# Kernel tuning notes

Hardware: AMD Instinct MI355X
Metric: run time of the kernel (lower is better)

The kernel has to match this reference:

```python
import jax, jax.numpy as jnp
import numpy as np

D_MODEL = 1024
NUM_HEADS = 16
D_HEAD = D_MODEL // NUM_HEADS
SCALE = float(np.sqrt(D_HEAD))
NEG = -1e9


def setup_inputs() -> dict:
    key = jax.random.key(0)
    ks = jax.random.split(key, 4)
    B, K = 4, 1024
    tokens = jax.random.normal(ks[0], (B, K, D_MODEL), dtype=jnp.float32)
    token_mask = jnp.ones((B, K), dtype=jnp.int32)
    W_qkv = jax.random.normal(ks[1], (D_MODEL, 3 * D_MODEL), dtype=jnp.float32) * 0.02
    b_qkv = jnp.zeros((3 * D_MODEL,), dtype=jnp.float32)
    W_proj = jax.random.normal(ks[2], (D_MODEL, D_MODEL), dtype=jnp.float32) * 0.02
    b_proj = jnp.zeros((D_MODEL,), dtype=jnp.float32)
    return {"tokens": tokens, "token_mask": token_mask, "W_qkv": W_qkv,
            "b_qkv": b_qkv, "W_proj": W_proj, "b_proj": b_proj}


def reference(tokens, token_mask, W_qkv, b_qkv, W_proj, b_proj):
    B, K, D = tokens.shape
    H, dh = NUM_HEADS, D // NUM_HEADS
    # QKV projection: (B, K, 3D) -> (3, B, H, K, dh)
    qkv = (tokens @ W_qkv + b_qkv).reshape(B, K, 3, H, dh)
    qkv = jnp.transpose(qkv, (2, 0, 3, 1, 4))
    q, k, v = qkv[0], qkv[1], qkv[2]
    # scaled scores (B, H, K, K)
    attn = jnp.einsum('bhqd,bhkd->bhqk', q, k) / SCALE
    # additive padding mask: valid iff both query and key positions valid
    tm = token_mask.astype(attn.dtype)
    m = tm[:, None, None, :] * tm[:, None, :, None]          # (B,1,K,K)
    attn = attn + (1.0 - jnp.clip(m, 0.0)) * NEG
    attn = jax.nn.softmax(attn, axis=-1)
    # weighted values, merge heads
    out = jnp.einsum('bhqk,bhkd->bhqd', attn, v)
    out = jnp.transpose(out, (0, 2, 1, 3)).reshape(B, K, D)
    out = out @ W_proj + b_proj
    tokens_out = tokens + out                                 # residual (dropout=0)
    attn_out = attn.mean(axis=1)                              # (B, K, K)
    return tokens_out, attn_out
```

## Files before the change

### kernel.cpp

```cpp
#include <hip/hip_runtime.h>
#include <hip/hip_bf16.h>
#include <math.h>

#define SEQ   1024
#define DM    1024
#define NH    16
#define DH    64
#define INV_SCALE 0.125f
#define NEGBIG   -1e9f
#define MASKPEN 80.0f

typedef __attribute__((ext_vector_type(8))) __bf16 bf16x8;
typedef __attribute__((ext_vector_type(4))) float floatx4;
typedef unsigned short ushort_t;

__device__ __forceinline__ floatx4 mfma16(bf16x8 a, bf16x8 b, floatx4 c) {
    return __builtin_amdgcn_mfma_f32_16x16x32_bf16(a, b, c, 0, 0, 0);
}

__device__ __forceinline__ ushort_t f2bf(float f) {
    unsigned int u = __float_as_uint(f);
    u += 0x7fffu + ((u >> 16) & 1u);
    return (ushort_t)(u >> 16);
}

__device__ __forceinline__ void gload_lds16(const void* g, void* l) {
    __builtin_amdgcn_global_load_lds(
        (const __attribute__((address_space(1))) unsigned int*)g,
        (__attribute__((address_space(3))) unsigned int*)l, 16, 0, 0);
}

__global__ __launch_bounds__(256) void k_prep(const float* __restrict__ tokens,
                                              ushort_t* __restrict__ Xbf,
                                              const float* __restrict__ Wqkv,
                                              ushort_t* __restrict__ Wt,
                                              const float* __restrict__ Wproj,
                                              ushort_t* __restrict__ Wpt) {
    __shared__ ushort_t tile[32][33];
    int bxg = blockIdx.x;
    if (bxg < 2048) {
        int i = (bxg * 256 + threadIdx.x) * 8;
        float4 a = *(const float4*)(tokens + i);
        float4 b = *(const float4*)(tokens + i + 4);
        union { ushort_t s[8]; uint4 v; } pk;
        pk.s[0] = f2bf(a.x); pk.s[1] = f2bf(a.y); pk.s[2] = f2bf(a.z); pk.s[3] = f2bf(a.w);
        pk.s[4] = f2bf(b.x); pk.s[5] = f2bf(b.y); pk.s[6] = f2bf(b.z); pk.s[7] = f2bf(b.w);
        *(uint4*)(Xbf + i) = pk.v;
        return;
    }
    const float* src; ushort_t* dst; int R, C, bx, by;
    if (bxg < 5120) {
        int idx = bxg - 2048;
        src = Wqkv; dst = Wt; R = DM; C = 3 * DM;
        bx = (idx % 96) * 32; by = (idx / 96) * 32;
    } else {
        int idx = bxg - 5120;
        src = Wproj; dst = Wpt; R = DM; C = DM;
        bx = (idx % 32) * 32; by = (idx / 32) * 32;
    }
    int tx = threadIdx.x & 31, ty = threadIdx.x >> 5;
    for (int i = ty; i < 32; i += 8)
        tile[i][tx] = f2bf(src[(size_t)(by + i) * C + bx + tx]);
    __syncthreads();
    for (int i = ty; i < 32; i += 8)
        dst[(size_t)(bx + i) * R + by + tx] = tile[tx][i];
}

__device__ __forceinline__ void gemm128_single(const ushort_t* __restrict__ A,
                                               const ushort_t* __restrict__ Bt,
                                               int m0, int n0, int Kd,
                                               floatx4 acc[4][4], ushort_t* smem) {
    int tid  = threadIdx.x;
    int wave = tid >> 6, lane = tid & 63;
    int l15 = lane & 15, quad = lane >> 4;
    int wr = (wave >> 1) * 64, wc = (wave & 1) * 64;
    int rsub = lane >> 2;
    int ksub = (((lane & 3) ^ ((lane >> 3) & 3)) * 8);
    int rsw  = (l15 >> 1) & 3;

    for (int k0 = 0; k0 < Kd; k0 += 32) {
        __syncthreads();
        #pragma unroll
        for (int c = 0; c < 2; ++c) {
            int rbase = wave * 32 + c * 16;
            gload_lds16(A  + (size_t)(m0 + rbase + rsub) * Kd + k0 + ksub,
                        smem + rbase * 32);
            gload_lds16(Bt + (size_t)(n0 + rbase + rsub) * Kd + k0 + ksub,
                        smem + 4096 + rbase * 32);
        }
        __syncthreads();

        bf16x8 af[4], bfr[4];
        #pragma unroll
        for (int i = 0; i < 4; ++i)
            af[i] = *(const bf16x8*)(smem + (wr + i * 16 + l15) * 32 + (quad ^ rsw) * 8);
        #pragma unroll
        for (int j = 0; j < 4; ++j)
            bfr[j] = *(const bf16x8*)(smem + 4096 + (wc + j * 16 + l15) * 32 + (quad ^ rsw) * 8);
        #pragma unroll
        for (int i = 0; i < 4; ++i)
            #pragma unroll
            for (int j = 0; j < 4; ++j)
                acc[i][j] = mfma16(af[i], bfr[j], acc[i][j]);
    }
}

__device__ __forceinline__ void gemm128_dbuf(const ushort_t* __restrict__ A,
                                             const ushort_t* __restrict__ Bt,
                                             int m0, int n0, int Kd,
                                             floatx4 acc[4][4], ushort_t* smem) {
    int tid  = threadIdx.x;
    int wave = tid >> 6, lane = tid & 63;
    int l15 = lane & 15, quad = lane >> 4;
    int wr = (wave >> 1) * 64, wc = (wave & 1) * 64;
    int rsub = lane >> 2;
    int ksub = (((lane & 3) ^ ((lane >> 3) & 3)) * 8);
    int rsw  = (l15 >> 1) & 3;

    #pragma unroll
    for (int c = 0; c < 2; ++c) {
        int rbase = wave * 32 + c * 16;
        gload_lds16(A  + (size_t)(m0 + rbase + rsub) * Kd + ksub,
                    smem + rbase * 32);
        gload_lds16(Bt + (size_t)(n0 + rbase + rsub) * Kd + ksub,
                    smem + 4096 + rbase * 32);
    }

    for (int k0 = 0; k0 < Kd; k0 += 32) {
        int sel = (k0 >> 5) & 1;
        ushort_t* cur = smem + sel * 8192;
        __syncthreads();
        if (k0 + 32 < Kd) {
            ushort_t* nxt = smem + (sel ^ 1) * 8192;
            #pragma unroll
            for (int c = 0; c < 2; ++c) {
                int rbase = wave * 32 + c * 16;
                gload_lds16(A  + (size_t)(m0 + rbase + rsub) * Kd + (k0 + 32) + ksub,
                            nxt + rbase * 32);
                gload_lds16(Bt + (size_t)(n0 + rbase + rsub) * Kd + (k0 + 32) + ksub,
                            nxt + 4096 + rbase * 32);
            }
        }

        bf16x8 af[4], bfr[4];
        #pragma unroll
        for (int i = 0; i < 4; ++i)
            af[i] = *(const bf16x8*)(cur + (wr + i * 16 + l15) * 32 + (quad ^ rsw) * 8);
        #pragma unroll
        for (int j = 0; j < 4; ++j)
            bfr[j] = *(const bf16x8*)(cur + 4096 + (wc + j * 16 + l15) * 32 + (quad ^ rsw) * 8);
        #pragma unroll
        for (int i = 0; i < 4; ++i)
            #pragma unroll
            for (int j = 0; j < 4; ++j)
                acc[i][j] = mfma16(af[i], bfr[j], acc[i][j]);
    }
}

__global__ __launch_bounds__(256, 2) void k_qkv_gemm(const ushort_t* __restrict__ X,
                                                     const ushort_t* __restrict__ Wt,
                                                     const float* __restrict__ bias,
                                                     ushort_t* __restrict__ qb,
                                                     ushort_t* __restrict__ kb,
                                                     ushort_t* __restrict__ vtb) {
    __shared__ ushort_t smem[16384];
    int m0 = blockIdx.y * 128, n0 = blockIdx.x * 128;
    floatx4 acc[4][4];
    #pragma unroll
    for (int i = 0; i < 4; ++i)
        #pragma unroll
        for (int j = 0; j < 4; ++j) acc[i][j] = (floatx4)0.0f;

    gemm128_dbuf(X, Wt, m0, n0, DM, acc, smem);

    int tid = threadIdx.x, wave = tid >> 6, lane = tid & 63;
    int l15 = lane & 15, quad = lane >> 4;
    int wr = (wave >> 1) * 64, wc = (wave & 1) * 64;
    #pragma unroll
    for (int i = 0; i < 4; ++i) {
        int mrow0 = m0 + wr + i * 16 + quad * 4;
        int b = mrow0 >> 10, t0 = mrow0 & 1023;
        #pragma unroll
        for (int j = 0; j < 4; ++j) {
            int n = n0 + wc + j * 16 + l15;
            float bv = bias[n];
            int sec = n >> 10, nn = n & 1023;
            int h = nn >> 6, d = nn & 63;
            if (sec == 2) {
                union { ushort_t s[4]; uint2 v; } pk;
                #pragma unroll
                for (int r = 0; r < 4; ++r) pk.s[r] = f2bf(acc[i][j][r] + bv);
                *(uint2*)(vtb + (((size_t)(b * NH + h) * DH + d) * SEQ + t0)) = pk.v;
            } else {
                ushort_t* dst = (sec == 0) ? qb : kb;
                #pragma unroll
                for (int r = 0; r < 4; ++r)
                    dst[((size_t)(b * NH + h) * SEQ + t0 + r) * DH + d] =
                        f2bf(acc[i][j][r] + bv);
            }
        }
    }
}

__global__ __launch_bounds__(256, 4) void k_attn_flash(const ushort_t* __restrict__ qb,
                                                       const ushort_t* __restrict__ kb,
                                                       const ushort_t* __restrict__ vtb,
                                                       const int* __restrict__ mask,
                                                       float* __restrict__ lbuf,
                                                       ushort_t* __restrict__ ob) {
    __shared__ ushort_t ks[2 * 64 * 64];
    __shared__ ushort_t vs[2 * 64 * 64];
    __shared__ ushort_t ps[4 * 16 * 64];
    int bh = blockIdx.x, qt = blockIdx.y;
    int b = bh >> 4, h = bh & 15;
    int tid = threadIdx.x, wave = tid >> 6, lane = tid & 63;
    int l15 = lane & 15, quad = lane >> 4;
    int qrow = qt * 64 + wave * 16;
    ushort_t* pw = ps + wave * 1024;
    int sw7 = l15 & 7;

    int srow = wave * 16 + (lane >> 3);
    int slog = (lane & 7) ^ (srow & 7);

    const ushort_t* qbase = qb + ((size_t)bh * SEQ + qrow + l15) * DH;
    bf16x8 aq0 = *(const bf16x8*)(qbase + quad * 8);
    bf16x8 aq1 = *(const bf16x8*)(qbase + 32 + quad * 8);

    bf16x8 vones;
    #pragma unroll
    for (int i = 0; i < 8; ++i) vones[i] = (__bf16)1.0f;

    float qp[4];
    #pragma unroll
    for (int r = 0; r < 4; ++r)
        qp[r] = MASKPEN * (float)mask[b * SEQ + qrow + quad * 4 + r];

    floatx4 oacc[4], lacc = (floatx4)0.0f;
    #pragma unroll
    for (int t = 0; t < 4; ++t) oacc[t] = (floatx4)0.0f;

    #pragma unroll
    for (int c = 0; c < 2; ++c) {
        gload_lds16(kb  + ((size_t)bh * SEQ + srow + c * 8) * DH + slog * 8,
                    ks + (wave * 16 + c * 8) * 64);
        gload_lds16(vtb + ((size_t)bh * DH + srow + c * 8) * SEQ + slog * 8,
                    vs + (wave * 16 + c * 8) * 64);
    }

    for (int it = 0; it < SEQ / 64; ++it) {
        int kc = it * 64;
        int sel = it & 1;
        __syncthreads();
        if (it + 1 < SEQ / 64) {
            int nsel = sel ^ 1;
            #pragma unroll
            for (int c = 0; c < 2; ++c) {
                gload_lds16(kb  + ((size_t)bh * SEQ + kc + 64 + srow + c * 8) * DH + slog * 8,
                            ks + nsel * 4096 + (wave * 16 + c * 8) * 64);
                gload_lds16(vtb + ((size_t)bh * DH + srow + c * 8) * SEQ + kc + 64 + slog * 8,
                            vs + nsel * 4096 + (wave * 16 + c * 8) * 64);
            }
        }
        const ushort_t* kcur = ks + sel * 4096;
        const ushort_t* vcur = vs + sel * 4096;

        floatx4 s[4];
        #pragma unroll
        for (int j = 0; j < 4; ++j) {
            int row = j * 16 + l15;
            bf16x8 k0 = *(const bf16x8*)(kcur + row * 64 + ((quad ^ sw7) * 8));
            bf16x8 k1 = *(const bf16x8*)(kcur + row * 64 + (((quad + 4) ^ sw7) * 8));
            s[j] = mfma16(aq0, k0, (floatx4)0.0f);
            s[j] = mfma16(aq1, k1, s[j]);
        }
        #pragma unroll
        for (int j = 0; j < 4; ++j) {
            float km = (float)mask[b * SEQ + kc + j * 16 + l15];
            #pragma unroll
            for (int r = 0; r < 4; ++r) {
                float arg = s[j][r] * INV_SCALE + (qp[r] * km - MASKPEN);
                float p = __expf(arg);
                int rd = quad * 4 + r;
                int ch = (2 * j + (l15 >> 3)) ^ (rd & 7);
                pw[rd * 64 + ch * 8 + (l15 & 7)] = f2bf(p);
            }
        }
        bf16x8 pa0 = *(const bf16x8*)(pw + l15 * 64 + ((quad ^ sw7) * 8));
        bf16x8 pa1 = *(const bf16x8*)(pw + l15 * 64 + (((quad + 4) ^ sw7) * 8));
        lacc = mfma16(pa0, vones, lacc);
        lacc = mfma16(pa1, vones, lacc);
        #pragma unroll
        for (int t = 0; t < 4; ++t) {
            bf16x8 bv0 = *(const bf16x8*)(vcur + (t * 16 + l15) * 64 + ((quad ^ sw7) * 8));
            bf16x8 bv1 = *(const bf16x8*)(vcur + (t * 16 + l15) * 64 + (((quad + 4) ^ sw7) * 8));
            oacc[t] = mfma16(pa0, bv0, oacc[t]);
            oacc[t] = mfma16(pa1, bv1, oacc[t]);
        }
    }
    float invl[4];
    #pragma unroll
    for (int r = 0; r < 4; ++r) invl[r] = 1.0f / lacc[r];
    #pragma unroll
    for (int t = 0; t < 4; ++t)
        #pragma unroll
        for (int r = 0; r < 4; ++r)
            ob[((size_t)b * SEQ + qrow + quad * 4 + r) * DM + h * DH + t * 16 + l15] =
                f2bf(oacc[t][r] * invl[r]);
    if (l15 == 0) {
        #pragma unroll
        for (int r = 0; r < 4; ++r)
            lbuf[(size_t)bh * SEQ + qrow + quad * 4 + r] = invl[r];
    }
}

__device__ __forceinline__ void proj_body(const ushort_t* __restrict__ ob,
                                          const ushort_t* __restrict__ Wpt,
                                          const float* __restrict__ bias,
                                          const float* __restrict__ tokens,
                                          float* __restrict__ out,
                                          int m0, int n0, ushort_t* smem) {
    floatx4 acc[4][4];
    #pragma unroll
    for (int i = 0; i < 4; ++i)
        #pragma unroll
        for (int j = 0; j < 4; ++j) acc[i][j] = (floatx4)0.0f;

    gemm128_single(ob, Wpt, m0, n0, DM, acc, smem);

    int tid = threadIdx.x, wave = tid >> 6, lane = tid & 63;
    int l15 = lane & 15, quad = lane >> 4;
    int wr = (wave >> 1) * 64, wc = (wave & 1) * 64;
    #pragma unroll
    for (int i = 0; i < 4; ++i) {
        int m0r = m0 + wr + i * 16 + quad * 4;
        #pragma unroll
        for (int j = 0; j < 4; ++j) {
            int n = n0 + wc + j * 16 + l15;
            float bv = bias[n];
            #pragma unroll
            for (int r = 0; r < 4; ++r) {
                size_t idx = (size_t)(m0r + r) * DM + n;
                out[idx] = acc[i][j][r] + bv + tokens[idx];
            }
        }
    }
}

__device__ __forceinline__ void avg_body(const ushort_t* __restrict__ qb,
                                         const ushort_t* __restrict__ kb,
                                         const int* __restrict__ mask,
                                         const float* __restrict__ lbuf,
                                         float* __restrict__ attn_out,
                                         int b, int qt, int kt, ushort_t* ks) {
    int tid = threadIdx.x, wave = tid >> 6, lane = tid & 63;
    int l15 = lane & 15, quad = lane >> 4;
    int q0 = qt * 64 + wave * 16;
    int kbase = kt * 64;
    int sw7 = l15 & 7;

    int srow = wave * 16 + (lane >> 3);
    int slog = (lane & 7) ^ (srow & 7);
    int bh0 = b * NH;

    float qp[4], km[4];
    #pragma unroll
    for (int r = 0; r < 4; ++r)
        qp[r] = MASKPEN * (float)mask[b * SEQ + q0 + quad * 4 + r];
    #pragma unroll
    for (int j = 0; j < 4; ++j)
        km[j] = (float)mask[b * SEQ + kbase + j * 16 + l15];

    floatx4 aacc[4];
    #pragma unroll
    for (int j = 0; j < 4; ++j) aacc[j] = (floatx4)0.0f;

    #pragma unroll
    for (int c = 0; c < 2; ++c)
        gload_lds16(kb + ((size_t)bh0 * SEQ + kbase + srow + c * 8) * DH + slog * 8,
                    ks + (wave * 16 + c * 8) * 64);
    const ushort_t* qp0 = qb + ((size_t)bh0 * SEQ + q0 + l15) * DH;
    bf16x8 aq0 = *(const bf16x8*)(qp0 + quad * 8);
    bf16x8 aq1 = *(const bf16x8*)(qp0 + 32 + quad * 8);
    floatx4 il = *(const floatx4*)(lbuf + (size_t)bh0 * SEQ + q0 + quad * 4);
    __syncthreads();

    for (int h = 0; h < NH; ++h) {
        ushort_t* cur = ks + (h & 1) * 4096;
        ushort_t* nxt = ks + ((h + 1) & 1) * 4096;
        if (h + 1 < NH) {
            #pragma unroll
            for (int c = 0; c < 2; ++c)
                gload_lds16(kb + ((size_t)(bh0 + h + 1) * SEQ + kbase + srow + c * 8) * DH + slog * 8,
                            nxt + (wave * 16 + c * 8) * 64);
        }
        bf16x8 caq0 = aq0, caq1 = aq1;
        floatx4 cil = il;
        if (h + 1 < NH) {
            const ushort_t* qpn = qb + ((size_t)(bh0 + h + 1) * SEQ + q0 + l15) * DH;
            aq0 = *(const bf16x8*)(qpn + quad * 8);
            aq1 = *(const bf16x8*)(qpn + 32 + quad * 8);
            il = *(const floatx4*)(lbuf + (size_t)(bh0 + h + 1) * SEQ + q0 + quad * 4);
        }
        cil *= 0.0625f;

        #pragma unroll
        for (int j = 0; j < 4; ++j) {
            int row = j * 16 + l15;
            bf16x8 k0 = *(const bf16x8*)(cur + row * 64 + ((quad ^ sw7) * 8));
            bf16x8 k1 = *(const bf16x8*)(cur + row * 64 + (((quad + 4) ^ sw7) * 8));
            floatx4 s = mfma16(caq0, k0, (floatx4)0.0f);
            s = mfma16(caq1, k1, s);
            #pragma unroll
            for (int r = 0; r < 4; ++r) {
                float arg = s[r] * INV_SCALE + (qp[r] * km[j] - MASKPEN);
                aacc[j][r] += __expf(arg) * cil[r];
            }
        }
        __syncthreads();
    }
    #pragma unroll
    for (int j = 0; j < 4; ++j)
        #pragma unroll
        for (int r = 0; r < 4; ++r)
            attn_out[((size_t)b * SEQ + q0 + quad * 4 + r) * SEQ +
                     kbase + j * 16 + l15] = aacc[j][r];
}

__global__ __launch_bounds__(256, 2) void k_proj_avg(const ushort_t* __restrict__ ob,
                                                     const ushort_t* __restrict__ Wpt,
                                                     const float* __restrict__ bias,
                                                     const float* __restrict__ tokens,
                                                     float* __restrict__ out,
                                                     const ushort_t* __restrict__ qb,
                                                     const ushort_t* __restrict__ kb,
                                                     const int* __restrict__ mask,
                                                     const float* __restrict__ lbuf,
                                                     float* __restrict__ attn_out) {
    __shared__ ushort_t smem[8192];
    int bxg = blockIdx.x;
    if (bxg < 256) {
        int xcd = bxg & 7, rank = bxg >> 3;
        int m = xcd * 4 + (rank >> 3);
        int n = rank & 7;
        proj_body(ob, Wpt, bias, tokens, out, m * 128, n * 128, smem);
    } else {
        int i = bxg - 256;
        int xcd = i & 7, rank = i >> 3;
        int b = rank >> 5;
        int r2 = rank & 31;
        int qt = (xcd >> 1) * 4 + (r2 >> 3);
        int kt = (xcd & 1) * 8 + (r2 & 7);
        avg_body(qb, kb, mask, lbuf, attn_out, b, qt, kt, smem);
    }
}

__global__ __launch_bounds__(256, 2) void k_proj(const ushort_t* __restrict__ ob,
                                                 const ushort_t* __restrict__ Wpt,
                                                 const float* __restrict__ bias,
                                                 const float* __restrict__ tokens,
                                                 float* __restrict__ out) {
    __shared__ ushort_t smem[8192];
    proj_body(ob, Wpt, bias, tokens, out, blockIdx.y * 128, blockIdx.x * 128, smem);
}

__global__ __launch_bounds__(256, 4) void k_attn_avg(const ushort_t* __restrict__ qb,
                                                     const ushort_t* __restrict__ kb,
                                                     const int* __restrict__ mask,
                                                     const float* __restrict__ lbuf,
                                                     float* __restrict__ attn_out) {
    __shared__ ushort_t ks[2 * 64 * 64];
    int i = blockIdx.x;
    int xcd = i & 7, rank = i >> 3;
    int b = rank >> 5;
    int r2 = rank & 31;
    int qt = (xcd >> 1) * 4 + (r2 >> 3);
    int kt = (xcd & 1) * 8 + (r2 & 7);
    avg_body(qb, kb, mask, lbuf, attn_out, b, qt, kt, ks);
}

extern "C" void kernel_launch(void* const* d_in, const int* in_sizes, int n_in,
                              void* d_out, int out_size, void* d_ws, size_t ws_size,
                              hipStream_t stream) {
    const float* tokens = (const float*)d_in[0];
    const int*   mask   = (const int*)d_in[1];
    const float* Wqkv   = (const float*)d_in[2];
    const float* bqkv   = (const float*)d_in[3];
    const float* Wproj  = (const float*)d_in[4];
    const float* bproj  = (const float*)d_in[5];

    float* out_tok  = (float*)d_out;
    float* out_attn = out_tok + (size_t)4 * SEQ * SEQ;

    ushort_t* Wt   = (ushort_t*)d_ws;
    ushort_t* Wpt  = Wt  + (size_t)3 * DM * DM;
    ushort_t* qbuf = Wpt + (size_t)DM * DM;
    ushort_t* kbuf = qbuf + (size_t)4 * SEQ * DM;
    ushort_t* vtb  = kbuf + (size_t)4 * SEQ * DM;
    float*    lbuf = (float*)(vtb + (size_t)4 * SEQ * DM);
    ushort_t* obuf_ws = (ushort_t*)(lbuf + (size_t)4 * NH * SEQ);
    const size_t WS_NEED = 42205184;

    bool big_ws = ws_size >= WS_NEED;
    ushort_t* Xbf  = (ushort_t*)out_attn;
    ushort_t* obuf = big_ws ? obuf_ws
                            : (ushort_t*)(out_attn + (size_t)2 * SEQ * SEQ);

    k_prep<<<6144, 256, 0, stream>>>(tokens, Xbf, Wqkv, Wt, Wproj, Wpt);
    k_qkv_gemm<<<dim3(24, 32), 256, 0, stream>>>(Xbf, Wt, bqkv, qbuf, kbuf, vtb);
    k_attn_flash<<<dim3(64, 16), 256, 0, stream>>>(qbuf, kbuf, vtb, mask, lbuf, obuf);
    if (big_ws) {
        k_proj_avg<<<256 + 1024, 256, 0, stream>>>(obuf, Wpt, bproj, tokens, out_tok,
                                                   qbuf, kbuf, mask, lbuf, out_attn);
    } else {
        k_proj<<<dim3(8, 32), 256, 0, stream>>>(obuf, Wpt, bproj, tokens, out_tok);
        k_attn_avg<<<1024, 256, 0, stream>>>(qbuf, kbuf, mask, lbuf, out_attn);
    }
}
```

Before: 199.0 us.

## Split fused proj/avg kernel and pipeline projection GEMM with 4-stage LDS buffering

Replaces the combined projection+attention-average kernel with separate launches, and rewrites the output projection GEMM as a standalone kernel using a 4-deep LDS ring buffer with explicit vmcnt waits so global loads for three future K-tiles are in flight during MFMA work. The XCD-aware tile mapping is kept. The intent is to hide load latency in the projection GEMM, which previously synced twice per K-step with a single buffer. The cost is 64KB of LDS per block (occupancy 1), and losing the concurrent overlap of projection and averaging blocks within one launch.

```diff
diff --git a/kernel.cpp b/kernel.cpp
--- a/kernel.cpp
+++ b/kernel.cpp
@@ -66,45 +66,6 @@
         dst[(size_t)(bx + i) * R + by + tx] = tile[tx][i];
 }
 
-__device__ __forceinline__ void gemm128_single(const ushort_t* __restrict__ A,
-                                               const ushort_t* __restrict__ Bt,
-                                               int m0, int n0, int Kd,
-                                               floatx4 acc[4][4], ushort_t* smem) {
-    int tid  = threadIdx.x;
-    int wave = tid >> 6, lane = tid & 63;
-    int l15 = lane & 15, quad = lane >> 4;
-    int wr = (wave >> 1) * 64, wc = (wave & 1) * 64;
-    int rsub = lane >> 2;
-    int ksub = (((lane & 3) ^ ((lane >> 3) & 3)) * 8);
-    int rsw  = (l15 >> 1) & 3;
-
-    for (int k0 = 0; k0 < Kd; k0 += 32) {
-        __syncthreads();
-        #pragma unroll
-        for (int c = 0; c < 2; ++c) {
-            int rbase = wave * 32 + c * 16;
-            gload_lds16(A  + (size_t)(m0 + rbase + rsub) * Kd + k0 + ksub,
-                        smem + rbase * 32);
-            gload_lds16(Bt + (size_t)(n0 + rbase + rsub) * Kd + k0 + ksub,
-                        smem + 4096 + rbase * 32);
-        }
-        __syncthreads();
-
-        bf16x8 af[4], bfr[4];
-        #pragma unroll
-        for (int i = 0; i < 4; ++i)
-            af[i] = *(const bf16x8*)(smem + (wr + i * 16 + l15) * 32 + (quad ^ rsw) * 8);
-        #pragma unroll
-        for (int j = 0; j < 4; ++j)
-            bfr[j] = *(const bf16x8*)(smem + 4096 + (wc + j * 16 + l15) * 32 + (quad ^ rsw) * 8);
-        #pragma unroll
-        for (int i = 0; i < 4; ++i)
-            #pragma unroll
-            for (int j = 0; j < 4; ++j)
-                acc[i][j] = mfma16(af[i], bfr[j], acc[i][j]);
-    }
-}
-
 __device__ __forceinline__ void gemm128_dbuf(const ushort_t* __restrict__ A,
                                              const ushort_t* __restrict__ Bt,
                                              int m0, int n0, int Kd,
@@ -313,23 +274,75 @@
     }
 }
 
-__device__ __forceinline__ void proj_body(const ushort_t* __restrict__ ob,
-                                          const ushort_t* __restrict__ Wpt,
-                                          const float* __restrict__ bias,
-                                          const float* __restrict__ tokens,
-                                          float* __restrict__ out,
-                                          int m0, int n0, ushort_t* smem) {
-    floatx4 acc[4][4];
-    #pragma unroll
-    for (int i = 0; i < 4; ++i)
-        #pragma unroll
-        for (int j = 0; j < 4; ++j) acc[i][j] = (floatx4)0.0f;
-
-    gemm128_single(ob, Wpt, m0, n0, DM, acc, smem);
-
-    int tid = threadIdx.x, wave = tid >> 6, lane = tid & 63;
+__device__ __forceinline__ void proj_stage(const ushort_t* __restrict__ ob,
+                                           const ushort_t* __restrict__ Wpt,
+                                           int m0, int n0, int t,
+                                           int wave, int rsub, int ksub,
+                                           ushort_t* buf) {
+    #pragma unroll
+    for (int c = 0; c < 2; ++c) {
+        int rbase = wave * 32 + c * 16;
+        gload_lds16(ob  + (size_t)(m0 + rbase + rsub) * DM + t * 32 + ksub,
+                    buf + rbase * 32);
+        gload_lds16(Wpt + (size_t)(n0 + rbase + rsub) * DM + t * 32 + ksub,
+                    buf + 4096 + rbase * 32);
+    }
+}
+
+__global__ __launch_bounds__(256, 1) void k_proj(const ushort_t* __restrict__ ob,
+                                                 const ushort_t* __restrict__ Wpt,
+                                                 const float* __restrict__ bias,
+                                                 const float* __restrict__ tokens,
+                                                 float* __restrict__ out) {
+    __shared__ ushort_t smem[4 * 8192];
+    int bxg = blockIdx.x;
+    int xcd = bxg & 7, rank = bxg >> 3;
+    int m0 = (xcd * 4 + (rank >> 3)) * 128;
+    int n0 = (rank & 7) * 128;
+
+    int tid  = threadIdx.x;
+    int wave = tid >> 6, lane = tid & 63;
     int l15 = lane & 15, quad = lane >> 4;
     int wr = (wave >> 1) * 64, wc = (wave & 1) * 64;
+    int rsub = lane >> 2;
+    int ksub = (((lane & 3) ^ ((lane >> 3) & 3)) * 8);
+    int rsw  = (l15 >> 1) & 3;
+
+    floatx4 acc[4][4];
+    #pragma unroll
+    for (int i = 0; i < 4; ++i)
+        #pragma unroll
+        for (int j = 0; j < 4; ++j) acc[i][j] = (floatx4)0.0f;
+
+    proj_stage(ob, Wpt, m0, n0, 0, wave, rsub, ksub, smem);
+    proj_stage(ob, Wpt, m0, n0, 1, wave, rsub, ksub, smem + 8192);
+    proj_stage(ob, Wpt, m0, n0, 2, wave, rsub, ksub, smem + 16384);
+
+    for (int t = 0; t < 32; ++t) {
+        __builtin_amdgcn_s_barrier();
+        if (t + 3 < 32)
+            proj_stage(ob, Wpt, m0, n0, t + 3, wave, rsub, ksub,
+                       smem + ((t + 3) & 3) * 8192);
+        if (t < 29)       asm volatile("s_waitcnt vmcnt(12)" ::: "memory");
+        else if (t == 29) asm volatile("s_waitcnt vmcnt(8)"  ::: "memory");
+        else if (t == 30) asm volatile("s_waitcnt vmcnt(4)"  ::: "memory");
+        else              asm volatile("s_waitcnt vmcnt(0)"  ::: "memory");
+
+        const ushort_t* cur = smem + (t & 3) * 8192;
+        bf16x8 af[4], bfr[4];
+        #pragma unroll
+        for (int i = 0; i < 4; ++i)
+            af[i] = *(const bf16x8*)(cur + (wr + i * 16 + l15) * 32 + (quad ^ rsw) * 8);
+        #pragma unroll
+        for (int j = 0; j < 4; ++j)
+            bfr[j] = *(const bf16x8*)(cur + 4096 + (wc + j * 16 + l15) * 32 + (quad ^ rsw) * 8);
+        #pragma unroll
+        for (int i = 0; i < 4; ++i)
+            #pragma unroll
+            for (int j = 0; j < 4; ++j)
+                acc[i][j] = mfma16(af[i], bfr[j], acc[i][j]);
+    }
+
     #pragma unroll
     for (int i = 0; i < 4; ++i) {
         int m0r = m0 + wr + i * 16 + quad * 4;
@@ -424,43 +437,6 @@
         for (int r = 0; r < 4; ++r)
             attn_out[((size_t)b * SEQ + q0 + quad * 4 + r) * SEQ +
                      kbase + j * 16 + l15] = aacc[j][r];
-}
-
-__global__ __launch_bounds__(256, 2) void k_proj_avg(const ushort_t* __restrict__ ob,
-                                                     const ushort_t* __restrict__ Wpt,
-                                                     const float* __restrict__ bias,
-                                                     const float* __restrict__ tokens,
-                                                     float* __restrict__ out,
-                                                     const ushort_t* __restrict__ qb,
-                                                     const ushort_t* __restrict__ kb,
-                                                     const int* __restrict__ mask,
-                                                     const float* __restrict__ lbuf,
-                                                     float* __restrict__ attn_out) {
-    __shared__ ushort_t smem[8192];
-    int bxg = blockIdx.x;
-    if (bxg < 256) {
-        int xcd = bxg & 7, rank = bxg >> 3;
-        int m = xcd * 4 + (rank >> 3);
-        int n = rank & 7;
-        proj_body(ob, Wpt, bias, tokens, out, m * 128, n * 128, smem);
-    } else {
-        int i = bxg - 256;
-        int xcd = i & 7, rank = i >> 3;
-        int b = rank >> 5;
-        int r2 = rank & 31;
-        int qt = (xcd >> 1) * 4 + (r2 >> 3);
-        int kt = (xcd & 1) * 8 + (r2 & 7);
-        avg_body(qb, kb, mask, lbuf, attn_out, b, qt, kt, smem);
-    }
-}
-
-__global__ __launch_bounds__(256, 2) void k_proj(const ushort_t* __restrict__ ob,
-                                                 const ushort_t* __restrict__ Wpt,
-                                                 const float* __restrict__ bias,
-                                                 const float* __restrict__ tokens,
-                                                 float* __restrict__ out) {
-    __shared__ ushort_t smem[8192];
-    proj_body(ob, Wpt, bias, tokens, out, blockIdx.y * 128, blockIdx.x * 128, smem);
 }
 
 __global__ __launch_bounds__(256, 4) void k_attn_avg(const ushort_t* __restrict__ qb,
@@ -508,11 +484,6 @@
     k_prep<<<6144, 256, 0, stream>>>(tokens, Xbf, Wqkv, Wt, Wproj, Wpt);
     k_qkv_gemm<<<dim3(24, 32), 256, 0, stream>>>(Xbf, Wt, bqkv, qbuf, kbuf, vtb);
     k_attn_flash<<<dim3(64, 16), 256, 0, stream>>>(qbuf, kbuf, vtb, mask, lbuf, obuf);
-    if (big_ws) {
-        k_proj_avg<<<256 + 1024, 256, 0, stream>>>(obuf, Wpt, bproj, tokens, out_tok,
-                                                   qbuf, kbuf, mask, lbuf, out_attn);
-    } else {
-        k_proj<<<dim3(8, 32), 256, 0, stream>>>(obuf, Wpt, bproj, tokens, out_tok);
-        k_attn_avg<<<1024, 256, 0, stream>>>(qbuf, kbuf, mask, lbuf, out_attn);
-    }
-}
+    k_proj<<<256, 256, 0, stream>>>(obuf, Wpt, bproj, tokens, out_tok);
+    k_attn_avg<<<1024, 256, 0, stream>>>(qbuf, kbuf, mask, lbuf, out_attn);
+}
```

Measured after the change: 200.4 us. No clear change (+0.7%).

## Deepen QKV GEMM LDS pipeline to four stages with explicit vmcnt waits

Applied to the files above, without the earlier changes.

Replaces the double-buffered QKV GEMM main loop with a 4-buffer ring that keeps three k-tiles of global-to-LDS loads in flight. It uses explicit s_waitcnt vmcnt counts and a raw s_barrier instead of __syncthreads. The goal is to hide more global memory latency behind MFMA work. LDS per block doubles to 64KB, which may limit occupancy at two blocks per CU, and the hand-tuned vmcnt counts rely on each stage issuing exactly four loads per thread.

```diff
diff --git a/kernel.cpp b/kernel.cpp
--- a/kernel.cpp
+++ b/kernel.cpp
@@ -105,10 +105,30 @@
     }
 }
 
-__device__ __forceinline__ void gemm128_dbuf(const ushort_t* __restrict__ A,
-                                             const ushort_t* __restrict__ Bt,
-                                             int m0, int n0, int Kd,
-                                             floatx4 acc[4][4], ushort_t* smem) {
+__device__ __forceinline__ void qkv_stage(const ushort_t* __restrict__ X,
+                                          const ushort_t* __restrict__ Wt,
+                                          int m0, int n0, int t,
+                                          int wave, int rsub, int ksub,
+                                          ushort_t* buf) {
+    #pragma unroll
+    for (int c = 0; c < 2; ++c) {
+        int rbase = wave * 32 + c * 16;
+        gload_lds16(X  + (size_t)(m0 + rbase + rsub) * DM + t * 32 + ksub,
+                    buf + rbase * 32);
+        gload_lds16(Wt + (size_t)(n0 + rbase + rsub) * DM + t * 32 + ksub,
+                    buf + 4096 + rbase * 32);
+    }
+}
+
+__global__ __launch_bounds__(256, 2) void k_qkv_gemm(const ushort_t* __restrict__ X,
+                                                     const ushort_t* __restrict__ Wt,
+                                                     const float* __restrict__ bias,
+                                                     ushort_t* __restrict__ qb,
+                                                     ushort_t* __restrict__ kb,
+                                                     ushort_t* __restrict__ vtb) {
+    __shared__ ushort_t smem[4 * 8192];
+    int m0 = blockIdx.y * 128, n0 = blockIdx.x * 128;
+
     int tid  = threadIdx.x;
     int wave = tid >> 6, lane = tid & 63;
     int l15 = lane & 15, quad = lane >> 4;
@@ -117,31 +137,26 @@
     int ksub = (((lane & 3) ^ ((lane >> 3) & 3)) * 8);
     int rsw  = (l15 >> 1) & 3;
 
-    #pragma unroll
-    for (int c = 0; c < 2; ++c) {
-        int rbase = wave * 32 + c * 16;
-        gload_lds16(A  + (size_t)(m0 + rbase + rsub) * Kd + ksub,
-                    smem + rbase * 32);
-        gload_lds16(Bt + (size_t)(n0 + rbase + rsub) * Kd + ksub,
-                    smem + 4096 + rbase * 32);
-    }
-
-    for (int k0 = 0; k0 < Kd; k0 += 32) {
-        int sel = (k0 >> 5) & 1;
-        ushort_t* cur = smem + sel * 8192;
-        __syncthreads();
-        if (k0 + 32 < Kd) {
-            ushort_t* nxt = smem + (sel ^ 1) * 8192;
-            #pragma unroll
-            for (int c = 0; c < 2; ++c) {
-                int rbase = wave * 32 + c * 16;
-                gload_lds16(A  + (size_t)(m0 + rbase + rsub) * Kd + (k0 + 32) + ksub,
-                            nxt + rbase * 32);
-                gload_lds16(Bt + (size_t)(n0 + rbase + rsub) * Kd + (k0 + 32) + ksub,
-                            nxt + 4096 + rbase * 32);
-            }
-        }
-
+    floatx4 acc[4][4];
+    #pragma unroll
+    for (int i = 0; i < 4; ++i)
+        #pragma unroll
+        for (int j = 0; j < 4; ++j) acc[i][j] = (floatx4)0.0f;
+
+    qkv_stage(X, Wt, m0, n0, 0, wave, rsub, ksub, smem);
+    qkv_stage(X, Wt, m0, n0, 1, wave, rsub, ksub, smem + 8192);
+    qkv_stage(X, Wt, m0, n0, 2, wave, rsub, ksub, smem + 16384);
+
+    for (int t = 0; t < 32; ++t) {
+        if (t < 30)       asm volatile("s_waitcnt vmcnt(8)" ::: "memory");
+        else if (t == 30) asm volatile("s_waitcnt vmcnt(4)" ::: "memory");
+        else              asm volatile("s_waitcnt vmcnt(0)" ::: "memory");
+        __builtin_amdgcn_s_barrier();
+        if (t + 3 < 32)
+            qkv_stage(X, Wt, m0, n0, t + 3, wave, rsub, ksub,
+                      smem + ((t + 3) & 3) * 8192);
+
+        const ushort_t* cur = smem + (t & 3) * 8192;
         bf16x8 af[4], bfr[4];
         #pragma unroll
         for (int i = 0; i < 4; ++i)
@@ -155,27 +170,7 @@
             for (int j = 0; j < 4; ++j)
                 acc[i][j] = mfma16(af[i], bfr[j], acc[i][j]);
     }
-}
-
-__global__ __launch_bounds__(256, 2) void k_qkv_gemm(const ushort_t* __restrict__ X,
-                                                     const ushort_t* __restrict__ Wt,
-                                                     const float* __restrict__ bias,
-                                                     ushort_t* __restrict__ qb,
-                                                     ushort_t* __restrict__ kb,
-                                                     ushort_t* __restrict__ vtb) {
-    __shared__ ushort_t smem[16384];
-    int m0 = blockIdx.y * 128, n0 = blockIdx.x * 128;
-    floatx4 acc[4][4];
-    #pragma unroll
-    for (int i = 0; i < 4; ++i)
-        #pragma unroll
-        for (int j = 0; j < 4; ++j) acc[i][j] = (floatx4)0.0f;
-
-    gemm128_dbuf(X, Wt, m0, n0, DM, acc, smem);
-
-    int tid = threadIdx.x, wave = tid >> 6, lane = tid & 63;
-    int l15 = lane & 15, quad = lane >> 4;
-    int wr = (wave >> 1) * 64, wc = (wave & 1) * 64;
+
     #pragma unroll
     for (int i = 0; i < 4; ++i) {
         int mrow0 = m0 + wr + i * 16 + quad * 4;
```

New measurement: 199.8 us. Within noise of the previous version (+0.4%).
